# Performance work log

Hardware: AMD Instinct MI355X
Metric: run time of the kernel (lower is better)

The kernel has to match this reference:

```python
import jax, jax.numpy as jnp
import numpy as np
import math

B, T, E, H = 8, 2048, 1024, 64  # batch, seq (== BLOCK_SIZE), emb_size, head_size


def setup_inputs() -> dict:
    key = jax.random.key(0)
    kx, kq, kk, kv = jax.random.split(key, 4)
    s = 1.0 / math.sqrt(E)
    return {
        "x": jax.random.normal(kx, (B, T, E), dtype=jnp.float32),
        "Wq": jax.random.uniform(kq, (H, E), dtype=jnp.float32, minval=-s, maxval=s),
        "Wk": jax.random.uniform(kk, (H, E), dtype=jnp.float32, minval=-s, maxval=s),
        "Wv": jax.random.uniform(kv, (H, E), dtype=jnp.float32, minval=-s, maxval=s),
        "should_mask": 1,
    }


def reference(x, Wq, Wk, Wv, should_mask):
    # Linear(E, H, bias=False): y = x @ W.T
    q = jnp.einsum("bte,he->bth", x, Wq)
    k = jnp.einsum("bte,he->bth", x, Wk)
    v = jnp.einsum("bte,he->bth", x, Wv)
    # NOTE: source multiplies by sqrt(head_size) (not the usual divide)
    affinity = jnp.einsum("bth,bsh->bts", q, k) * jnp.float32(math.sqrt(H))
    if should_mask:
        tril = jnp.tril(jnp.ones((T, T), dtype=bool))
        affinity = jnp.where(tril, affinity, jnp.float32(-jnp.inf))
    weight = jax.nn.softmax(affinity, axis=-1)
    # dropout omitted (eval mode) for determinism
    out = jnp.einsum("bts,bsh->bth", weight, v)
    return out
```

## Files before the change

### kernel.cpp

```cpp
#include <hip/hip_runtime.h>
#include <math.h>

#define NB 8
#define NT 2048
#define NE 1024
#define NH 64

typedef __attribute__((ext_vector_type(8))) short bh8;
typedef __attribute__((ext_vector_type(4))) float f4;

typedef unsigned short u16;

__device__ __forceinline__ u16 bf16rn(float f) {
    unsigned u = __float_as_uint(f);
    u += 0x7FFFu + ((u >> 16) & 1u);
    return (u16)(u >> 16);
}
__device__ __forceinline__ float bf16f(u16 h) {
    return __uint_as_float(((unsigned)h) << 16);
}
__device__ __forceinline__ int swzq(int quad, int row) {
    return ((quad ^ (row & 7)) << 3);
}

__global__ void wprep(const float* __restrict__ wq, const float* __restrict__ wk,
                      const float* __restrict__ wv,
                      u16* __restrict__ whi, u16* __restrict__ wlo)
{
    const int row = blockIdx.x;
    const int k0  = threadIdx.x * 4;
    const float* src = (row < 64)  ? (wq + (size_t)row * NE)
                     : (row < 128) ? (wk + (size_t)(row - 64) * NE)
                     :               (wv + (size_t)(row - 128) * NE);
    float4 v = *(const float4*)(src + k0);
    ushort4 h, l;
    h.x = bf16rn(v.x); l.x = bf16rn(v.x - bf16f(h.x));
    h.y = bf16rn(v.y); l.y = bf16rn(v.y - bf16f(h.y));
    h.z = bf16rn(v.z); l.z = bf16rn(v.z - bf16f(h.z));
    h.w = bf16rn(v.w); l.w = bf16rn(v.w - bf16f(h.w));
    const int c   = k0 >> 6;
    const int kk  = k0 & 63;
    const int pos = c * 64 + swzq(kk >> 3, row) + (kk & 7);
    *(ushort4*)(whi + (size_t)row * NE + pos) = h;
    *(ushort4*)(wlo + (size_t)row * NE + pos) = l;
}

__global__ __launch_bounds__(256, 2) void qkv_mfma(
    const float* __restrict__ x, const u16* __restrict__ whi_, const u16* __restrict__ wlo_,
    u16* __restrict__ qhi, u16* __restrict__ qlo,
    u16* __restrict__ khi, u16* __restrict__ klo, u16* __restrict__ vtp)
{
    __shared__ u16 xh[32][64], xl[32][64];
    __shared__ u16 wh[192][64], wl[192][64];

    const int tid  = threadIdx.x;
    const int wid  = tid >> 6;
    const int lane = tid & 63;
    const int t15  = lane & 15, t4 = lane >> 4;
    const int row0 = blockIdx.x * 32;

    const f4 fzero = {0.f, 0.f, 0.f, 0.f};
    f4 acc[2][3];
#pragma unroll
    for (int m = 0; m < 2; ++m)
#pragma unroll
        for (int n = 0; n < 3; ++n) acc[m][n] = fzero;

    for (int kt = 0; kt < NE; kt += 64) {
        __syncthreads();
#pragma unroll
        for (int it = 0; it < 2; ++it) {
            const int f = tid + it * 256;
            const int r = f >> 4, k0 = (f & 15) * 4;
            float4 v = *(const float4*)(x + (size_t)(row0 + r) * NE + kt + k0);
            ushort4 h, l;
            h.x = bf16rn(v.x); l.x = bf16rn(v.x - bf16f(h.x));
            h.y = bf16rn(v.y); l.y = bf16rn(v.y - bf16f(h.y));
            h.z = bf16rn(v.z); l.z = bf16rn(v.z - bf16f(h.z));
            h.w = bf16rn(v.w); l.w = bf16rn(v.w - bf16f(h.w));
            const int pos = swzq(k0 >> 3, r) + (k0 & 7);
            *(ushort4*)&xh[r][pos] = h;
            *(ushort4*)&xl[r][pos] = l;
        }
#pragma unroll
        for (int it = 0; it < 6; ++it) {
            const int f = tid + it * 256;
            const int r = f >> 3, sg = f & 7;
            *(uint4*)&wh[r][sg * 8] = *(const uint4*)(whi_ + (size_t)r * NE + kt + sg * 8);
            *(uint4*)&wl[r][sg * 8] = *(const uint4*)(wlo_ + (size_t)r * NE + kt + sg * 8);
        }
        __syncthreads();

#pragma unroll
        for (int ks = 0; ks < 2; ++ks) {
            const int quad = 4 * ks + t4;
            bh8 ah[2], al[2];
#pragma unroll
            for (int m = 0; m < 2; ++m) {
                const int r = m * 16 + t15;
                ah[m] = *(const bh8*)&xh[r][swzq(quad, r)];
                al[m] = *(const bh8*)&xl[r][swzq(quad, r)];
            }
#pragma unroll
            for (int n = 0; n < 3; ++n) {
                const int c = wid * 48 + n * 16 + t15;
                bh8 bhv = *(const bh8*)&wh[c][swzq(quad, c)];
                bh8 blv = *(const bh8*)&wl[c][swzq(quad, c)];
#pragma unroll
                for (int m = 0; m < 2; ++m) {
                    acc[m][n] = __builtin_amdgcn_mfma_f32_16x16x32_bf16(ah[m], bhv, acc[m][n], 0, 0, 0);
                    acc[m][n] = __builtin_amdgcn_mfma_f32_16x16x32_bf16(ah[m], blv, acc[m][n], 0, 0, 0);
                    acc[m][n] = __builtin_amdgcn_mfma_f32_16x16x32_bf16(al[m], bhv, acc[m][n], 0, 0, 0);
                }
            }
        }
    }

#pragma unroll
    for (int m = 0; m < 2; ++m) {
#pragma unroll
        for (int n = 0; n < 3; ++n) {
            const int col = wid * 48 + n * 16 + t15;
#pragma unroll
            for (int r = 0; r < 4; ++r) {
                const int row = row0 + m * 16 + t4 * 4 + r;
                float v = acc[m][n][r];
                if (col < 64) {
                    v *= 8.0f;
                    const u16 h = bf16rn(v);
                    const int pos = swzq(col >> 3, row) + (col & 7);
                    qhi[(size_t)row * NH + pos] = h;
                    qlo[(size_t)row * NH + pos] = bf16rn(v - bf16f(h));
                } else if (col < 128) {
                    const int cc  = col - 64;
                    const u16 h = bf16rn(v);
                    const int pos = swzq(cc >> 3, row) + (cc & 7);
                    khi[(size_t)row * NH + pos] = h;
                    klo[(size_t)row * NH + pos] = bf16rn(v - bf16f(h));
                } else {
                    const int hh  = col - 128;
                    const int b   = row >> 11;
                    const int tok = row & (NT - 1);
                    const int c   = tok & 63;
                    const int p   = (c & 15) * 4 + (c >> 4);
                    const int tp  = (tok & ~63) | (swzq(p >> 3, hh) + (p & 7));
                    vtp[((size_t)b * NH + hh) * NT + tp] = bf16rn(v);
                }
            }
        }
    }
}

__global__ __launch_bounds__(256, 2) void attn_mfma(
    const u16* __restrict__ qhi, const u16* __restrict__ qlo,
    const u16* __restrict__ khi, const u16* __restrict__ klo,
    const u16* __restrict__ vtp, const int* __restrict__ smp,
    float* __restrict__ out,
    float* __restrict__ po, float* __restrict__ pm, float* __restrict__ pl)
{
    __shared__ u16 kh[64][64], kl[64][64], vt[64][64], ps[64][64];

    const int tid  = threadIdx.x;
    const int wid  = tid >> 6;
    const int lane = tid & 63;
    const int t15  = lane & 15, t4 = lane >> 4;
    const int b    = blockIdx.y;
    const int u    = 79 - (int)blockIdx.x;
    int qt, c;
    if (u < 8)       { qt = u;                   c = 0; }
    else if (u < 24) { qt = 8  + ((u - 8) >> 1); c = (u - 8) & 1; }
    else if (u < 48) { qt = 16 + (u - 24) / 3;   c = (u - 24) % 3; }
    else             { qt = 24 + ((u - 48) >> 2); c = (u - 48) & 3; }
    const int nch   = (qt + 8) >> 3;
    const int sm    = smp[0];
    const int total = sm ? (qt + 1) : (NT / 64);
    const int jt0   = c * total / nch;
    const int jt1   = (c + 1) * total / nch;
    const int qs    = qt * 64;

    const size_t bb = (size_t)b * NT;

    bh8 qh[2], ql[2];
#pragma unroll
    for (int ks = 0; ks < 2; ++ks) {
        const size_t off = (bb + qs + wid * 16 + t15) * NH + swzq(4 * ks + t4, t15);
        qh[ks] = *(const bh8*)(qhi + off);
        ql[ks] = *(const bh8*)(qlo + off);
    }

    const f4 fzero = {0.f, 0.f, 0.f, 0.f};
    f4 o[4];
    float m_i[4], l_i[4];
#pragma unroll
    for (int i = 0; i < 4; ++i) { o[i] = fzero; m_i[i] = -INFINITY; l_i[i] = 0.f; }

    for (int jt = jt0; jt < jt1; ++jt) {
        const int js = jt * 64;
        __syncthreads();
#pragma unroll
        for (int it = 0; it < 2; ++it) {
            const int f = tid + it * 256;
            const int r = f >> 3, sg = f & 7;
            *(uint4*)&kh[r][sg * 8] = *(const uint4*)(khi + (bb + js + r) * NH + sg * 8);
            *(uint4*)&kl[r][sg * 8] = *(const uint4*)(klo + (bb + js + r) * NH + sg * 8);
            *(uint4*)&vt[r][sg * 8] = *(const uint4*)(vtp + ((size_t)b * NH + r) * NT + js + sg * 8);
        }
        __syncthreads();

        f4 s[4];
#pragma unroll
        for (int n = 0; n < 4; ++n) s[n] = fzero;
#pragma unroll
        for (int n = 0; n < 4; ++n) {
#pragma unroll
            for (int ks = 0; ks < 2; ++ks) {
                const int rr = n * 16 + t15;
                bh8 bhv = *(const bh8*)&kh[rr][swzq(4 * ks + t4, rr)];
                bh8 blv = *(const bh8*)&kl[rr][swzq(4 * ks + t4, rr)];
                s[n] = __builtin_amdgcn_mfma_f32_16x16x32_bf16(qh[ks], bhv, s[n], 0, 0, 0);
                s[n] = __builtin_amdgcn_mfma_f32_16x16x32_bf16(qh[ks], blv, s[n], 0, 0, 0);
                s[n] = __builtin_amdgcn_mfma_f32_16x16x32_bf16(ql[ks], bhv, s[n], 0, 0, 0);
            }
        }

        if (sm && jt == qt) {
#pragma unroll
            for (int n = 0; n < 4; ++n) {
                const int col = n * 16 + t15;
#pragma unroll
                for (int r = 0; r < 4; ++r)
                    if (col > wid * 16 + t4 * 4 + r) s[n][r] = -INFINITY;
            }
        }

#pragma unroll
        for (int r = 0; r < 4; ++r) {
            float rm = fmaxf(fmaxf(s[0][r], s[1][r]), fmaxf(s[2][r], s[3][r]));
            rm = fmaxf(rm, __shfl_xor(rm, 1));
            rm = fmaxf(rm, __shfl_xor(rm, 2));
            rm = fmaxf(rm, __shfl_xor(rm, 4));
            rm = fmaxf(rm, __shfl_xor(rm, 8));
            const float mn = fmaxf(m_i[r], rm);
            const float cf = __expf(m_i[r] - mn);
            const float p0 = __expf(s[0][r] - mn);
            const float p1 = __expf(s[1][r] - mn);
            const float p2 = __expf(s[2][r] - mn);
            const float p3 = __expf(s[3][r] - mn);
            float rs = p0 + p1 + p2 + p3;
            rs += __shfl_xor(rs, 1);
            rs += __shfl_xor(rs, 2);
            rs += __shfl_xor(rs, 4);
            rs += __shfl_xor(rs, 8);
            l_i[r] = l_i[r] * cf + rs;
            m_i[r] = mn;
#pragma unroll
            for (int hs = 0; hs < 4; ++hs) o[hs][r] *= cf;
            ushort4 pw;
            pw.x = bf16rn(p0); pw.y = bf16rn(p1); pw.z = bf16rn(p2); pw.w = bf16rn(p3);
            const int R = wid * 16 + t4 * 4 + r;
            *(ushort4*)&ps[R][swzq(t15 >> 1, R) + (t15 & 1) * 4] = pw;
        }

#pragma unroll
        for (int ks = 0; ks < 2; ++ks) {
            const int pr = wid * 16 + t15;
            bh8 pa = *(const bh8*)&ps[pr][swzq(4 * ks + t4, pr)];
#pragma unroll
            for (int hs = 0; hs < 4; ++hs) {
                const int vr = hs * 16 + t15;
                bh8 bv = *(const bh8*)&vt[vr][swzq(4 * ks + t4, vr)];
                o[hs] = __builtin_amdgcn_mfma_f32_16x16x32_bf16(pa, bv, o[hs], 0, 0, 0);
            }
        }
    }

    if (nch == 1) {
#pragma unroll
        for (int r = 0; r < 4; ++r) {
            const float inv = 1.0f / l_i[r];
            const size_t rowoff = (bb + qs + wid * 16 + t4 * 4 + r) * NH;
#pragma unroll
            for (int hs = 0; hs < 4; ++hs)
                out[rowoff + hs * 16 + t15] = o[hs][r] * inv;
        }
    } else {
        const int slot = (b * 24 + (qt - 8)) * 4 + c;
        float* pop = po + (size_t)slot * 64 * 64;
#pragma unroll
        for (int r = 0; r < 4; ++r) {
            const int rl = wid * 16 + t4 * 4 + r;
#pragma unroll
            for (int hs = 0; hs < 4; ++hs)
                pop[(size_t)rl * 64 + hs * 16 + t15] = o[hs][r];
            if (t15 == 0) {
                pm[(size_t)slot * 64 + rl] = m_i[r];
                pl[(size_t)slot * 64 + rl] = l_i[r];
            }
        }
    }
}

__global__ void attn_combine(const float* __restrict__ po, const float* __restrict__ pm,
                             const float* __restrict__ pl, float* __restrict__ out)
{
    const int qt  = 8 + (int)blockIdx.x;
    const int b   = blockIdx.y;
    const int nch = (qt + 8) >> 3;
    const int tid = threadIdx.x;
    const int r   = tid >> 2;
    const int h0  = (tid & 3) * 16;
    const int base = (b * 24 + (qt - 8)) * 4;

    float m[4], w[4];
    float M = -INFINITY;
#pragma unroll
    for (int cc = 0; cc < 4; ++cc) {
        m[cc] = (cc < nch) ? pm[(size_t)(base + cc) * 64 + r] : -INFINITY;
        M = fmaxf(M, m[cc]);
    }
    float denom = 0.f;
#pragma unroll
    for (int cc = 0; cc < 4; ++cc) {
        w[cc] = (cc < nch) ? __expf(m[cc] - M) : 0.f;
        denom += ((cc < nch) ? pl[(size_t)(base + cc) * 64 + r] : 0.f) * w[cc];
    }
    const float inv = 1.0f / denom;

    const size_t orow = ((size_t)b * NT + (size_t)qt * 64 + r) * NH;
#pragma unroll
    for (int v = 0; v < 4; ++v) {
        float4 acc = make_float4(0.f, 0.f, 0.f, 0.f);
#pragma unroll
        for (int cc = 0; cc < 4; ++cc) {
            if (cc < nch) {
                float4 pv = *(const float4*)(po + ((size_t)(base + cc) * 64 + r) * 64 + h0 + v * 4);
                acc.x += pv.x * w[cc]; acc.y += pv.y * w[cc];
                acc.z += pv.z * w[cc]; acc.w += pv.w * w[cc];
            }
        }
        acc.x *= inv; acc.y *= inv; acc.z *= inv; acc.w *= inv;
        *(float4*)(out + orow + h0 + v * 4) = acc;
    }
}

extern "C" void kernel_launch(void* const* d_in, const int* in_sizes, int n_in,
                              void* d_out, int out_size, void* d_ws, size_t ws_size,
                              hipStream_t stream)
{
    const float* x  = (const float*)d_in[0];
    const float* wq = (const float*)d_in[1];
    const float* wk = (const float*)d_in[2];
    const float* wv = (const float*)d_in[3];
    const int*   sm = (const int*)d_in[4];
    float* out = (float*)d_out;

    u16* whi = (u16*)d_ws;
    u16* wlo = whi + (size_t)192 * NE;
    u16* qhi = wlo + (size_t)192 * NE;
    u16* qlo = qhi + (size_t)NB * NT * NH;
    u16* khi = qlo + (size_t)NB * NT * NH;
    u16* klo = khi + (size_t)NB * NT * NH;
    u16* vtp = klo + (size_t)NB * NT * NH;
    float* po = (float*)(vtp + (size_t)NB * NT * NH);
    float* pm = po + (size_t)NB * 24 * 4 * 64 * 64;
    float* pl = pm + (size_t)NB * 24 * 4 * 64;

    wprep<<<dim3(192), 256, 0, stream>>>(wq, wk, wv, whi, wlo);
    qkv_mfma<<<dim3((NB * NT) / 32), 256, 0, stream>>>(x, whi, wlo, qhi, qlo, khi, klo, vtp);
    attn_mfma<<<dim3(80, NB), 256, 0, stream>>>(qhi, qlo, khi, klo, vtp, sm, out, po, pm, pl);
    attn_combine<<<dim3(24, NB), 256, 0, stream>>>(po, pm, pl, out);
}
```

Measured before the change: 159.5 us.

## Double-buffer QKV and attention tiles with async global-to-LDS loads

The QKV projection kernel now processes 64-row tiles instead of 32. It double-buffers the x and weight tiles in shared memory, with weights loaded straight into LDS by global_load_lds and the next x tile prefetched into registers during compute. The attention kernel likewise double-buffers its K and V tiles, issuing async direct-to-LDS loads for the next tile while computing on the current one. The aim is to hide global memory latency behind MFMA work. In exchange, the QKV kernel's LDS footprint grows to about 128KB and it drops to one block per CU, so less latency can be hidden by running several blocks at once.

```diff
diff --git a/kernel.cpp b/kernel.cpp
--- a/kernel.cpp
+++ b/kernel.cpp
@@ -21,6 +21,11 @@
 }
 __device__ __forceinline__ int swzq(int quad, int row) {
     return ((quad ^ (row & 7)) << 3);
+}
+__device__ __forceinline__ void gll16(const u16* g, u16* l) {
+    __builtin_amdgcn_global_load_lds(
+        (const __attribute__((address_space(1))) unsigned int*)g,
+        (__attribute__((address_space(3))) unsigned int*)l, 16, 0, 0);
 }
 
 __global__ void wprep(const float* __restrict__ wq, const float* __restrict__ wk,
@@ -45,79 +50,110 @@
     *(ushort4*)(wlo + (size_t)row * NE + pos) = l;
 }
 
-__global__ __launch_bounds__(256, 2) void qkv_mfma(
+__global__ __launch_bounds__(256, 1) void qkv_mfma(
     const float* __restrict__ x, const u16* __restrict__ whi_, const u16* __restrict__ wlo_,
     u16* __restrict__ qhi, u16* __restrict__ qlo,
     u16* __restrict__ khi, u16* __restrict__ klo, u16* __restrict__ vtp)
 {
-    __shared__ u16 xh[32][64], xl[32][64];
-    __shared__ u16 wh[192][64], wl[192][64];
+    __shared__ u16 xh[2][64][64], xl[2][64][64];
+    __shared__ u16 wh[2][192][64], wl[2][192][64];
 
     const int tid  = threadIdx.x;
     const int wid  = tid >> 6;
     const int lane = tid & 63;
     const int t15  = lane & 15, t4 = lane >> 4;
-    const int row0 = blockIdx.x * 32;
-
-    const f4 fzero = {0.f, 0.f, 0.f, 0.f};
-    f4 acc[2][3];
-#pragma unroll
-    for (int m = 0; m < 2; ++m)
-#pragma unroll
-        for (int n = 0; n < 3; ++n) acc[m][n] = fzero;
-
-    for (int kt = 0; kt < NE; kt += 64) {
-        __syncthreads();
-#pragma unroll
-        for (int it = 0; it < 2; ++it) {
+    const int row0 = blockIdx.x * 64;
+
+    auto stageW = [&](int buf, int kt) {
+#pragma unroll
+        for (int it = 0; it < 6; ++it) {
+            const int f = tid + it * 256;
+            const int r = f >> 3, sg = f & 7;
+            const size_t go = (size_t)r * NE + kt + sg * 8;
+            u16* lb_h = &wh[buf][0][0] + (size_t)(wid * 64 + it * 256) * 8;
+            u16* lb_l = &wl[buf][0][0] + (size_t)(wid * 64 + it * 256) * 8;
+            gll16(whi_ + go, lb_h);
+            gll16(wlo_ + go, lb_l);
+        }
+    };
+    auto loadX = [&](int kt, float4* xr) {
+#pragma unroll
+        for (int it = 0; it < 4; ++it) {
             const int f = tid + it * 256;
             const int r = f >> 4, k0 = (f & 15) * 4;
-            float4 v = *(const float4*)(x + (size_t)(row0 + r) * NE + kt + k0);
+            xr[it] = *(const float4*)(x + (size_t)(row0 + r) * NE + kt + k0);
+        }
+    };
+    auto writeX = [&](int buf, const float4* xr) {
+#pragma unroll
+        for (int it = 0; it < 4; ++it) {
+            const int f = tid + it * 256;
+            const int r = f >> 4, k0 = (f & 15) * 4;
+            const float4 v = xr[it];
             ushort4 h, l;
             h.x = bf16rn(v.x); l.x = bf16rn(v.x - bf16f(h.x));
             h.y = bf16rn(v.y); l.y = bf16rn(v.y - bf16f(h.y));
             h.z = bf16rn(v.z); l.z = bf16rn(v.z - bf16f(h.z));
             h.w = bf16rn(v.w); l.w = bf16rn(v.w - bf16f(h.w));
             const int pos = swzq(k0 >> 3, r) + (k0 & 7);
-            *(ushort4*)&xh[r][pos] = h;
-            *(ushort4*)&xl[r][pos] = l;
-        }
-#pragma unroll
-        for (int it = 0; it < 6; ++it) {
-            const int f = tid + it * 256;
-            const int r = f >> 3, sg = f & 7;
-            *(uint4*)&wh[r][sg * 8] = *(const uint4*)(whi_ + (size_t)r * NE + kt + sg * 8);
-            *(uint4*)&wl[r][sg * 8] = *(const uint4*)(wlo_ + (size_t)r * NE + kt + sg * 8);
-        }
-        __syncthreads();
+            *(ushort4*)&xh[buf][r][pos] = h;
+            *(ushort4*)&xl[buf][r][pos] = l;
+        }
+    };
+
+    const f4 fzero = {0.f, 0.f, 0.f, 0.f};
+    f4 acc[4][3];
+#pragma unroll
+    for (int m = 0; m < 4; ++m)
+#pragma unroll
+        for (int n = 0; n < 3; ++n) acc[m][n] = fzero;
+
+    {
+        float4 xr[4];
+        loadX(0, xr);
+        stageW(0, 0);
+        writeX(0, xr);
+    }
+    __syncthreads();
+
+    for (int t = 0; t < 16; ++t) {
+        const int c = t & 1, nb = c ^ 1;
+        float4 xr[4];
+        if (t < 15) {
+            loadX((t + 1) * 64, xr);
+            stageW(nb, (t + 1) * 64);
+        }
 
 #pragma unroll
         for (int ks = 0; ks < 2; ++ks) {
             const int quad = 4 * ks + t4;
-            bh8 ah[2], al[2];
-#pragma unroll
-            for (int m = 0; m < 2; ++m) {
+            bh8 ah[4], al[4];
+#pragma unroll
+            for (int m = 0; m < 4; ++m) {
                 const int r = m * 16 + t15;
-                ah[m] = *(const bh8*)&xh[r][swzq(quad, r)];
-                al[m] = *(const bh8*)&xl[r][swzq(quad, r)];
+                ah[m] = *(const bh8*)&xh[c][r][swzq(quad, r)];
+                al[m] = *(const bh8*)&xl[c][r][swzq(quad, r)];
             }
 #pragma unroll
             for (int n = 0; n < 3; ++n) {
-                const int c = wid * 48 + n * 16 + t15;
-                bh8 bhv = *(const bh8*)&wh[c][swzq(quad, c)];
-                bh8 blv = *(const bh8*)&wl[c][swzq(quad, c)];
-#pragma unroll
-                for (int m = 0; m < 2; ++m) {
+                const int cc = wid * 48 + n * 16 + t15;
+                bh8 bhv = *(const bh8*)&wh[c][cc][swzq(quad, cc)];
+                bh8 blv = *(const bh8*)&wl[c][cc][swzq(quad, cc)];
+#pragma unroll
+                for (int m = 0; m < 4; ++m) {
                     acc[m][n] = __builtin_amdgcn_mfma_f32_16x16x32_bf16(ah[m], bhv, acc[m][n], 0, 0, 0);
                     acc[m][n] = __builtin_amdgcn_mfma_f32_16x16x32_bf16(ah[m], blv, acc[m][n], 0, 0, 0);
                     acc[m][n] = __builtin_amdgcn_mfma_f32_16x16x32_bf16(al[m], bhv, acc[m][n], 0, 0, 0);
                 }
             }
         }
-    }
-
-#pragma unroll
-    for (int m = 0; m < 2; ++m) {
+
+        if (t < 15) writeX(nb, xr);
+        __syncthreads();
+    }
+
+#pragma unroll
+    for (int m = 0; m < 4; ++m) {
 #pragma unroll
         for (int n = 0; n < 3; ++n) {
             const int col = wid * 48 + n * 16 + t15;
@@ -141,8 +177,8 @@
                     const int hh  = col - 128;
                     const int b   = row >> 11;
                     const int tok = row & (NT - 1);
-                    const int c   = tok & 63;
-                    const int p   = (c & 15) * 4 + (c >> 4);
+                    const int cv  = tok & 63;
+                    const int p   = (cv & 15) * 4 + (cv >> 4);
                     const int tp  = (tok & ~63) | (swzq(p >> 3, hh) + (p & 7));
                     vtp[((size_t)b * NH + hh) * NT + tp] = bf16rn(v);
                 }
@@ -158,7 +194,8 @@
     float* __restrict__ out,
     float* __restrict__ po, float* __restrict__ pm, float* __restrict__ pl)
 {
-    __shared__ u16 kh[64][64], kl[64][64], vt[64][64], ps[64][64];
+    __shared__ u16 kh[2][64][64], kl[2][64][64], vt[2][64][64];
+    __shared__ u16 ps[64][64];
 
     const int tid  = threadIdx.x;
     const int wid  = tid >> 6;
@@ -180,6 +217,22 @@
 
     const size_t bb = (size_t)b * NT;
 
+    auto stageKV = [&](int buf, int js) {
+#pragma unroll
+        for (int it = 0; it < 2; ++it) {
+            const int f = tid + it * 256;
+            const int r = f >> 3, sg = f & 7;
+            const size_t ck = (bb + js + r) * (size_t)NH + sg * 8;
+            const size_t cv = ((size_t)b * NH + r) * NT + js + sg * 8;
+            u16* lk = &kh[buf][0][0] + (size_t)(wid * 64 + it * 256) * 8;
+            u16* ll = &kl[buf][0][0] + (size_t)(wid * 64 + it * 256) * 8;
+            u16* lv = &vt[buf][0][0] + (size_t)(wid * 64 + it * 256) * 8;
+            gll16(khi + ck, lk);
+            gll16(klo + ck, ll);
+            gll16(vtp + cv, lv);
+        }
+    };
+
     bh8 qh[2], ql[2];
 #pragma unroll
     for (int ks = 0; ks < 2; ++ks) {
@@ -194,18 +247,12 @@
 #pragma unroll
     for (int i = 0; i < 4; ++i) { o[i] = fzero; m_i[i] = -INFINITY; l_i[i] = 0.f; }
 
+    stageKV(0, jt0 * 64);
+    __syncthreads();
+
+    int cur = 0;
     for (int jt = jt0; jt < jt1; ++jt) {
-        const int js = jt * 64;
-        __syncthreads();
-#pragma unroll
-        for (int it = 0; it < 2; ++it) {
-            const int f = tid + it * 256;
-            const int r = f >> 3, sg = f & 7;
-            *(uint4*)&kh[r][sg * 8] = *(const uint4*)(khi + (bb + js + r) * NH + sg * 8);
-            *(uint4*)&kl[r][sg * 8] = *(const uint4*)(klo + (bb + js + r) * NH + sg * 8);
-            *(uint4*)&vt[r][sg * 8] = *(const uint4*)(vtp + ((size_t)b * NH + r) * NT + js + sg * 8);
-        }
-        __syncthreads();
+        if (jt + 1 < jt1) stageKV(cur ^ 1, (jt + 1) * 64);
 
         f4 s[4];
 #pragma unroll
@@ -215,8 +262,8 @@
 #pragma unroll
             for (int ks = 0; ks < 2; ++ks) {
                 const int rr = n * 16 + t15;
-                bh8 bhv = *(const bh8*)&kh[rr][swzq(4 * ks + t4, rr)];
-                bh8 blv = *(const bh8*)&kl[rr][swzq(4 * ks + t4, rr)];
+                bh8 bhv = *(const bh8*)&kh[cur][rr][swzq(4 * ks + t4, rr)];
+                bh8 blv = *(const bh8*)&kl[cur][rr][swzq(4 * ks + t4, rr)];
                 s[n] = __builtin_amdgcn_mfma_f32_16x16x32_bf16(qh[ks], bhv, s[n], 0, 0, 0);
                 s[n] = __builtin_amdgcn_mfma_f32_16x16x32_bf16(qh[ks], blv, s[n], 0, 0, 0);
                 s[n] = __builtin_amdgcn_mfma_f32_16x16x32_bf16(ql[ks], bhv, s[n], 0, 0, 0);
@@ -268,10 +315,13 @@
 #pragma unroll
             for (int hs = 0; hs < 4; ++hs) {
                 const int vr = hs * 16 + t15;
-                bh8 bv = *(const bh8*)&vt[vr][swzq(4 * ks + t4, vr)];
+                bh8 bv = *(const bh8*)&vt[cur][vr][swzq(4 * ks + t4, vr)];
                 o[hs] = __builtin_amdgcn_mfma_f32_16x16x32_bf16(pa, bv, o[hs], 0, 0, 0);
             }
         }
+
+        __syncthreads();
+        cur ^= 1;
     }
 
     if (nch == 1) {
@@ -366,7 +416,7 @@
     float* pl = pm + (size_t)NB * 24 * 4 * 64;
 
     wprep<<<dim3(192), 256, 0, stream>>>(wq, wk, wv, whi, wlo);
-    qkv_mfma<<<dim3((NB * NT) / 32), 256, 0, stream>>>(x, whi, wlo, qhi, qlo, khi, klo, vtp);
+    qkv_mfma<<<dim3((NB * NT) / 64), 256, 0, stream>>>(x, whi, wlo, qhi, qlo, khi, klo, vtp);
     attn_mfma<<<dim3(80, NB), 256, 0, stream>>>(qhi, qlo, khi, klo, vtp, sm, out, po, pm, pl);
     attn_combine<<<dim3(24, NB), 256, 0, stream>>>(po, pm, pl, out);
 }
```

New measurement: 174.4 us. 9.4% more time.
